# Kernel optimization log

Measured on AMD Instinct MI355X. Metric: run time of the kernel, lower is better.

The kernel has to match this reference:

```python
import jax, jax.numpy as jnp
import numpy as np

LN_EPS = 1e-5


def layer_norm(x, gamma, beta):
    mu = jnp.mean(x, axis=-1, keepdims=True)
    var = jnp.mean(jnp.square(x - mu), axis=-1, keepdims=True)
    return (x - mu) * jax.lax.rsqrt(var + LN_EPS) * gamma + beta


def setup_inputs() -> dict:
    key = jax.random.key(0)
    ks = jax.random.split(key, 7)
    B, S, D = 8, 1024, 512
    H, Dh = 8, 64
    scale = 1.0 / np.sqrt(D)
    x = jax.random.normal(ks[0], (B, S, D), dtype=jnp.float32)
    Wq = jax.random.normal(ks[1], (D, H * Dh), dtype=jnp.float32) * scale
    Wk = jax.random.normal(ks[2], (D, H * Dh), dtype=jnp.float32) * scale
    Wv = jax.random.normal(ks[3], (D, H * Dh), dtype=jnp.float32) * scale
    Wfc = jax.random.normal(ks[4], (H * Dh, D), dtype=jnp.float32) * scale
    gamma = jnp.ones((D,), dtype=jnp.float32)
    beta = jnp.zeros((D,), dtype=jnp.float32)
    return {"x": x, "Wq": Wq, "Wk": Wk, "Wv": Wv, "Wfc": Wfc, "gamma": gamma, "beta": beta}


def reference(x, Wq, Wk, Wv, Wfc, gamma, beta):
    B, S, D = x.shape
    H, Dh = 8, 64
    Q = (x @ Wq).reshape(B, S, H, Dh).transpose(0, 2, 1, 3)  # [B,H,S,Dh]
    K = (x @ Wk).reshape(B, S, H, Dh).transpose(0, 2, 1, 3)
    V = (x @ Wv).reshape(B, S, H, Dh).transpose(0, 2, 1, 3)
    scores = jnp.einsum('bhqd,bhkd->bhqk', Q, K) / np.sqrt(Dh).astype(np.float32)
    # tridiagonal band mask; NOTE: original fills off-band with -1e-09 (not -inf)
    idx = jnp.arange(S)
    band = jnp.abs(idx[:, None] - idx[None, :]) <= 1  # [S,S]
    scores = jnp.where(band, scores, jnp.float32(-1e-09))
    attn = jax.nn.softmax(scores, axis=-1)
    context = jnp.einsum('bhqk,bhkd->bhqd', attn, V)  # [B,H,S,Dh]
    context = context.transpose(0, 2, 1, 3).reshape(B, S, H * Dh)
    out = context @ Wfc
    return layer_norm(out + x, gamma, beta)
```

## Files before the change

### kernel.cpp

```cpp
#include <hip/hip_runtime.h>
#include <math.h>


typedef short     s8v  __attribute__((ext_vector_type(8)));
typedef float     f4v  __attribute__((ext_vector_type(4)));
typedef unsigned short us4v __attribute__((ext_vector_type(4)));
typedef unsigned short us8v __attribute__((ext_vector_type(8)));

__device__ __forceinline__ unsigned short f2b(float f) {
  union { float f; unsigned int u; } v; v.f = f;
  unsigned int u = v.u;
  return (unsigned short)((u + 0x7fffu + ((u >> 16) & 1u)) >> 16);
}
__device__ __forceinline__ float b2f(unsigned short u) {
  union { unsigned int i; float f; } v; v.i = ((unsigned int)u) << 16;
  return v.f;
}
__device__ __forceinline__ void gload_lds16(const void* g, void* l) {
  __builtin_amdgcn_global_load_lds(
      (const __attribute__((address_space(1))) void*)g,
      (__attribute__((address_space(3))) void*)l, 16, 0, 0);
}

__global__ __launch_bounds__(256) void conv_kernel(
    const float* __restrict__ x,
    const float* __restrict__ Wq, const float* __restrict__ Wk,
    const float* __restrict__ Wv, const float* __restrict__ Wfc,
    unsigned short* __restrict__ xb, unsigned short* __restrict__ Wt,
    float* __restrict__ Vsum) {
  __shared__ unsigned short tile[32][33];
  const int bid = blockIdx.x, t = threadIdx.x;
  if (bid < 4096) {
    const int i = bid * 256 + t;
    const float4 f = ((const float4*)x)[i];
    us4v o; o[0] = f2b(f.x); o[1] = f2b(f.y); o[2] = f2b(f.z); o[3] = f2b(f.w);
    ((us4v*)xb)[i] = o;
  } else if (bid < 5120) {
    const int id = bid - 4096;
    const int z = id >> 8, rem = id & 255;
    const int bx = rem & 15, by = rem >> 4;
    const float* W = (z == 0) ? Wq : (z == 1) ? Wk : (z == 2) ? Wv : Wfc;
    const int tx = t & 31, ty = t >> 5;
    const int n0 = bx * 32, k0 = by * 32;
    #pragma unroll
    for (int r = ty; r < 32; r += 8)
      tile[r][tx] = f2b(W[(size_t)(k0 + r) * 512 + n0 + tx]);
    __syncthreads();
    unsigned short* dst = Wt + (size_t)z * 512 * 512;
    #pragma unroll
    for (int r = ty; r < 32; r += 8)
      dst[(size_t)(n0 + r) * 512 + k0 + tx] = tile[tx][r];
  } else {
    float4 zz = {0.f, 0.f, 0.f, 0.f};
    #pragma unroll
    for (int p = 0; p < 4; ++p) ((float4*)Vsum)[p * 256 + t] = zz;
  }
}

#define BM 128
#define BN 128
#define BK 32

__global__ __launch_bounds__(256) void gemm_qkv_kernel(
    const unsigned short* __restrict__ A, const unsigned short* __restrict__ Bt,
    unsigned short* __restrict__ C, float* __restrict__ Vsum) {
  const int M = 8192, N = 1536, K = 512;
  __shared__ __align__(16) unsigned short smem[16384];
  unsigned short* As = smem;
  unsigned short* Bs = smem + 4096;
  const int t    = threadIdx.x;
  const int wave = t >> 6, lane = t & 63;
  const int wr   = wave >> 1, wc = wave & 1;
  const int quad = lane >> 4, l16 = lane & 15;
  const int bm = blockIdx.y * BM, bn = blockIdx.x * BN;

  const int ci0 = wave * 128 + lane, ci1 = ci0 + 64;
  const int r0 = ci0 >> 2, c0 = (ci0 & 3) ^ ((r0 >> 1) & 3);
  const int r1 = ci1 >> 2, c1 = (ci1 & 3) ^ ((r1 >> 1) & 3);
  const unsigned short* ga0 = A  + (size_t)(bm + r0) * K + c0 * 8;
  const unsigned short* ga1 = A  + (size_t)(bm + r1) * K + c1 * 8;
  const unsigned short* gb0 = Bt + (size_t)(bn + r0) * K + c0 * 8;
  const unsigned short* gb1 = Bt + (size_t)(bn + r1) * K + c1 * 8;
  unsigned short* la0 = As + wave * 1024;
  unsigned short* la1 = As + wave * 1024 + 512;
  unsigned short* lb0 = Bs + wave * 1024;
  unsigned short* lb1 = Bs + wave * 1024 + 512;

  const int sw = (l16 >> 1) & 3;

  f4v acc[4][4];
  #pragma unroll
  for (int i = 0; i < 4; ++i)
    #pragma unroll
    for (int j = 0; j < 4; ++j) {
      f4v z = {0.f, 0.f, 0.f, 0.f};
      acc[i][j] = z;
    }

  for (int kt = 0; kt < K; kt += BK) {
    gload_lds16(ga0 + kt, la0);
    gload_lds16(ga1 + kt, la1);
    gload_lds16(gb0 + kt, lb0);
    gload_lds16(gb1 + kt, lb1);
    __syncthreads();

    s8v af[4], bf[4];
    #pragma unroll
    for (int i = 0; i < 4; ++i) {
      const int r = wr * 64 + i * 16 + l16;
      af[i] = *(const s8v*)&As[(r * 4 + (quad ^ sw)) * 8];
    }
    #pragma unroll
    for (int j = 0; j < 4; ++j) {
      const int r = wc * 64 + j * 16 + l16;
      bf[j] = *(const s8v*)&Bs[(r * 4 + (quad ^ sw)) * 8];
    }
    #pragma unroll
    for (int i = 0; i < 4; ++i)
      #pragma unroll
      for (int j = 0; j < 4; ++j)
        acc[i][j] = __builtin_amdgcn_mfma_f32_16x16x32_bf16(
            af[i], bf[j], acc[i][j], 0, 0, 0);
    __syncthreads();
  }

  if (bn >= 1024) {
    const int b = bm >> 10;
    #pragma unroll
    for (int j = 0; j < 4; ++j) {
      float ps = 0.f;
      #pragma unroll
      for (int i = 0; i < 4; ++i)
        #pragma unroll
        for (int r = 0; r < 4; ++r) ps += acc[i][j][r];
      ps += __shfl_xor(ps, 16);
      ps += __shfl_xor(ps, 32);
      if (quad == 0)
        atomicAdd(&Vsum[b * 512 + (bn - 1024) + wc * 64 + j * 16 + l16], ps);
    }
  }

  #pragma unroll
  for (int i = 0; i < 4; ++i) {
    const int lr0 = wr * 64 + i * 16 + quad * 4;
    #pragma unroll
    for (int j = 0; j < 4; ++j) {
      const int lc = wc * 64 + j * 16 + l16;
      #pragma unroll
      for (int r = 0; r < 4; ++r)
        smem[(lr0 + r) * 128 + lc] = f2b(acc[i][j][r]);
    }
  }
  __syncthreads();
  #pragma unroll
  for (int p = 0; p < 8; ++p) {
    const int row = p * 16 + (t >> 4);
    const int ch  = t & 15;
    *(us8v*)(C + (size_t)(bm + row) * N + bn + ch * 8) =
        *(const us8v*)&smem[row * 128 + ch * 8];
  }
}

#define KVS 68
__global__ __launch_bounds__(256) void attn_kernel(
    const unsigned short* __restrict__ QKV, const float* __restrict__ Vsum,
    unsigned short* __restrict__ ctx) {
  __shared__ __align__(16) unsigned short Ks[130 * KVS];
  __shared__ __align__(16) unsigned short Vs[130 * KVS];
  __shared__ __align__(16) float vs_s[64];
  const int bh = blockIdx.x;
  const int b = bh >> 3, h = bh & 7;
  const int q0 = blockIdx.y * 128;
  const int t = threadIdx.x;
  const size_t rowb = ((size_t)b * 1024) * 1536;

  #pragma unroll
  for (int p = 0; p < 5; ++p) {
    const int i = p * 32 + (t >> 3);
    if (i < 130) {
      int g = q0 - 1 + i;
      g = g < 0 ? 0 : (g > 1023 ? 1023 : g);
      const unsigned short* src =
          QKV + rowb + (size_t)g * 1536 + h * 64 + (t & 7) * 8;
      const us8v kv = *(const us8v*)(src + 512);
      const us8v vv = *(const us8v*)(src + 1024);
      us4v lo, hi;
      #pragma unroll
      for (int r = 0; r < 4; ++r) { lo[r] = kv[r]; hi[r] = kv[r + 4]; }
      *(us4v*)&Ks[i * KVS + (t & 7) * 8]     = lo;
      *(us4v*)&Ks[i * KVS + (t & 7) * 8 + 4] = hi;
      #pragma unroll
      for (int r = 0; r < 4; ++r) { lo[r] = vv[r]; hi[r] = vv[r + 4]; }
      *(us4v*)&Vs[i * KVS + (t & 7) * 8]     = lo;
      *(us4v*)&Vs[i * KVS + (t & 7) * 8 + 4] = hi;
    }
  }
  if (t < 64) vs_s[t] = Vsum[(b << 9) + h * 64 + t];
  __syncthreads();

  const int q    = q0 + (t >> 1);
  const int half = t & 1;
  const int li   = (t >> 1) + 1;
  const int co   = half * 32;

  float pm = 0.f, p0 = 0.f, pp = 0.f;
  const unsigned short* Qp = QKV + rowb + (size_t)q * 1536 + h * 64 + co;
  const us8v qa = *(const us8v*)(Qp);
  const us8v qb = *(const us8v*)(Qp + 8);
  const us8v qc = *(const us8v*)(Qp + 16);
  const us8v qd = *(const us8v*)(Qp + 24);
  #pragma unroll
  for (int jj = 0; jj < 8; ++jj) {
    const us4v km = *(const us4v*)&Ks[(li - 1) * KVS + co + jj * 4];
    const us4v k0 = *(const us4v*)&Ks[li * KVS + co + jj * 4];
    const us4v kp = *(const us4v*)&Ks[(li + 1) * KVS + co + jj * 4];
    #pragma unroll
    for (int r = 0; r < 4; ++r) {
      const int e = jj * 4 + r;
      const unsigned short qu = (e < 8) ? qa[e & 7] : (e < 16) ? qb[e & 7]
                              : (e < 24) ? qc[e & 7] : qd[e & 7];
      const float qf = b2f(qu);
      pm += qf * b2f(km[r]);
      p0 += qf * b2f(k0[r]);
      pp += qf * b2f(kp[r]);
    }
  }
  pm += __shfl_xor(pm, 1);
  p0 += __shfl_xor(p0, 1);
  pp += __shfl_xor(pp, 1);

  const float OFF = -1e-9f;
  const float s0 = p0 * 0.125f;
  const float sm = (q > 0)    ? pm * 0.125f : OFF;
  const float sp = (q < 1023) ? pp * 0.125f : OFF;
  const float m  = fmaxf(fmaxf(s0, sm), fmaxf(sp, OFF));
  const float e0 = __expf(s0 - m), em = __expf(sm - m), ep = __expf(sp - m);
  const float eoff = __expf(OFF - m);
  const float inv  = 1.f / (e0 + em + ep + 1021.f * eoff);
  const float wm = (em - eoff) * inv, w0 = (e0 - eoff) * inv,
              wp = (ep - eoff) * inv, wt = eoff * inv;

  unsigned short* cp = ctx + ((size_t)(b * 1024 + q)) * 512 + h * 64 + co;
  #pragma unroll
  for (int jj = 0; jj < 8; ++jj) {
    const us4v a  = *(const us4v*)&Vs[(li - 1) * KVS + co + jj * 4];
    const us4v v0 = *(const us4v*)&Vs[li * KVS + co + jj * 4];
    const us4v c  = *(const us4v*)&Vs[(li + 1) * KVS + co + jj * 4];
    const float4 vsv = *(const float4*)&vs_s[co + jj * 4];
    us4v o;
    o[0] = f2b(wt * vsv.x + wm * b2f(a[0]) + w0 * b2f(v0[0]) + wp * b2f(c[0]));
    o[1] = f2b(wt * vsv.y + wm * b2f(a[1]) + w0 * b2f(v0[1]) + wp * b2f(c[1]));
    o[2] = f2b(wt * vsv.z + wm * b2f(a[2]) + w0 * b2f(v0[2]) + wp * b2f(c[2]));
    o[3] = f2b(wt * vsv.w + wm * b2f(a[3]) + w0 * b2f(v0[3]) + wp * b2f(c[3]));
    *(us4v*)(cp + jj * 4) = o;
  }
}

#define OS 516

__global__ __launch_bounds__(512) void gemm_fcln_kernel(
    const unsigned short* __restrict__ A,
    const unsigned short* __restrict__ Bt,
    const float* __restrict__ x, const float* __restrict__ gamma,
    const float* __restrict__ beta, float* __restrict__ y) {
  const int K = 512;
  __shared__ __align__(16) char smemraw[32 * OS * 4];
  unsigned short* As = (unsigned short*)smemraw;
  unsigned short* Bs = As + 1024;
  float* outS = (float*)smemraw;

  const int t    = threadIdx.x;
  const int wave = t >> 6, lane = t & 63;
  const int wrr  = wave >> 2, wcc = wave & 3;
  const int quad = lane >> 4, l16 = lane & 15;
  const int bm = blockIdx.x * 32;
  const int sw = (l16 >> 1) & 3;

  const int cia = wave * 64 + lane;
  const int ra = cia >> 2, ca = (cia & 3) ^ ((ra >> 1) & 3);
  const unsigned short* gA = A + (size_t)(bm + ra) * K + ca * 8;
  unsigned short* lA = As + wave * 512;
  int rb[4], cb[4];
  #pragma unroll
  for (int p = 0; p < 4; ++p) {
    const int ci = wave * 256 + p * 64 + lane;
    rb[p] = ci >> 2; cb[p] = (ci & 3) ^ ((rb[p] >> 1) & 3);
  }
  unsigned short* lB = Bs + wave * 2048;

  f4v acc[8];
  #pragma unroll
  for (int j = 0; j < 8; ++j) {
    f4v z = {0.f, 0.f, 0.f, 0.f};
    acc[j] = z;
  }

  for (int kt = 0; kt < K; kt += BK) {
    if (wave < 2) gload_lds16(gA + kt, lA);
    #pragma unroll
    for (int p = 0; p < 4; ++p)
      gload_lds16(Bt + (size_t)rb[p] * K + kt + cb[p] * 8, lB + p * 512);
    __syncthreads();

    const int rm = wrr * 16 + l16;
    const s8v af = *(const s8v*)&As[(rm * 4 + (quad ^ sw)) * 8];
    #pragma unroll
    for (int j = 0; j < 8; ++j) {
      const int n = wcc * 128 + j * 16 + l16;
      const s8v bf = *(const s8v*)&Bs[(n * 4 + (quad ^ sw)) * 8];
      acc[j] = __builtin_amdgcn_mfma_f32_16x16x32_bf16(af, bf, acc[j], 0, 0, 0);
    }
    __syncthreads();
  }

  #pragma unroll
  for (int j = 0; j < 8; ++j) {
    const int col = wcc * 128 + j * 16 + l16;
    const int row0 = wrr * 16 + quad * 4;
    #pragma unroll
    for (int r = 0; r < 4; ++r)
      outS[(row0 + r) * OS + col] = acc[j][r];
  }
  __syncthreads();

  const int row = t >> 4, l = t & 15;
  const size_t gbase = (size_t)(bm + row) * 512;
  float4 v[8];
  float s1 = 0.f, s2 = 0.f;
  #pragma unroll
  for (int k = 0; k < 8; ++k) {
    const int c = k * 64 + l * 4;
    const float4 a  = *(const float4*)&outS[row * OS + c];
    const float4 xv = *(const float4*)&x[gbase + c];
    float4 w;
    w.x = a.x + xv.x; w.y = a.y + xv.y; w.z = a.z + xv.z; w.w = a.w + xv.w;
    v[k] = w;
    s1 += w.x + w.y + w.z + w.w;
    s2 += w.x * w.x + w.y * w.y + w.z * w.z + w.w * w.w;
  }
  #pragma unroll
  for (int m = 1; m < 16; m <<= 1) {
    s1 += __shfl_xor(s1, m);
    s2 += __shfl_xor(s2, m);
  }
  const float mu  = s1 * (1.f / 512.f);
  const float var = s2 * (1.f / 512.f) - mu * mu;
  const float rs  = rsqrtf(var + 1e-5f);
  #pragma unroll
  for (int k = 0; k < 8; ++k) {
    const int c = k * 64 + l * 4;
    const float4 g  = *(const float4*)&gamma[c];
    const float4 bb = *(const float4*)&beta[c];
    float4 o;
    o.x = (v[k].x - mu) * rs * g.x + bb.x;
    o.y = (v[k].y - mu) * rs * g.y + bb.y;
    o.z = (v[k].z - mu) * rs * g.z + bb.z;
    o.w = (v[k].w - mu) * rs * g.w + bb.w;
    *(float4*)&y[gbase + c] = o;
  }
}

extern "C" void kernel_launch(void* const* d_in, const int* in_sizes, int n_in,
                              void* d_out, int out_size, void* d_ws, size_t ws_size,
                              hipStream_t stream) {
  const float* x     = (const float*)d_in[0];
  const float* Wq    = (const float*)d_in[1];
  const float* Wk    = (const float*)d_in[2];
  const float* Wv    = (const float*)d_in[3];
  const float* Wfc   = (const float*)d_in[4];
  const float* gamma = (const float*)d_in[5];
  const float* beta  = (const float*)d_in[6];
  float* y = (float*)d_out;

  char* ws = (char*)d_ws;
  unsigned short* Wt   = (unsigned short*)(ws);
  unsigned short* xb   = (unsigned short*)(ws + 2097152);
  unsigned short* QKV  = (unsigned short*)(ws + 10485760);
  float*          Vsum = (float*)(ws + 35651584);
  unsigned short* ctx  = (unsigned short*)(ws + 35667968);

  conv_kernel<<<5121, 256, 0, stream>>>(x, Wq, Wk, Wv, Wfc, xb, Wt, Vsum);
  gemm_qkv_kernel<<<dim3(12, 64), 256, 0, stream>>>(xb, Wt, QKV, Vsum);
  attn_kernel<<<dim3(64, 8), 256, 0, stream>>>(QKV, Vsum, ctx);
  gemm_fcln_kernel<<<256, 512, 0, stream>>>(
      ctx, Wt + (size_t)1536 * 512, x, gamma, beta, y);
}
```

Measured before the change: 136.8 us.

## Widen GEMM K tiles, double-buffer fc GEMM, stage Q in LDS, bf16 residual

Result: faster. 128.1 us (-6.4%).

```diff
diff --git a/kernel.cpp b/kernel.cpp
--- a/kernel.cpp
+++ b/kernel.cpp
@@ -57,36 +57,26 @@
   }
 }
 
-#define BM 128
-#define BN 128
-#define BK 32
-
 __global__ __launch_bounds__(256) void gemm_qkv_kernel(
     const unsigned short* __restrict__ A, const unsigned short* __restrict__ Bt,
     unsigned short* __restrict__ C, float* __restrict__ Vsum) {
-  const int M = 8192, N = 1536, K = 512;
+  const int N = 1536, K = 512;
   __shared__ __align__(16) unsigned short smem[16384];
   unsigned short* As = smem;
-  unsigned short* Bs = smem + 4096;
-  const int t    = threadIdx.x;
-  const int wave = t >> 6, lane = t & 63;
-  const int wr   = wave >> 1, wc = wave & 1;
+  unsigned short* Bs = smem + 8192;
+  const int t = threadIdx.x, wave = t >> 6, lane = t & 63;
+  const int wr = wave >> 1, wc = wave & 1;
   const int quad = lane >> 4, l16 = lane & 15;
-  const int bm = blockIdx.y * BM, bn = blockIdx.x * BN;
-
-  const int ci0 = wave * 128 + lane, ci1 = ci0 + 64;
-  const int r0 = ci0 >> 2, c0 = (ci0 & 3) ^ ((r0 >> 1) & 3);
-  const int r1 = ci1 >> 2, c1 = (ci1 & 3) ^ ((r1 >> 1) & 3);
-  const unsigned short* ga0 = A  + (size_t)(bm + r0) * K + c0 * 8;
-  const unsigned short* ga1 = A  + (size_t)(bm + r1) * K + c1 * 8;
-  const unsigned short* gb0 = Bt + (size_t)(bn + r0) * K + c0 * 8;
-  const unsigned short* gb1 = Bt + (size_t)(bn + r1) * K + c1 * 8;
-  unsigned short* la0 = As + wave * 1024;
-  unsigned short* la1 = As + wave * 1024 + 512;
-  unsigned short* lb0 = Bs + wave * 1024;
-  unsigned short* lb1 = Bs + wave * 1024 + 512;
-
-  const int sw = (l16 >> 1) & 3;
+  const int bm = blockIdx.y * 128, bn = blockIdx.x * 128;
+
+  const unsigned short *gA[4], *gB[4];
+  #pragma unroll
+  for (int p = 0; p < 4; ++p) {
+    const int ci = wave * 256 + p * 64 + lane;
+    const int r = ci >> 3, c = (ci & 7) ^ (r & 7);
+    gA[p] = A + (size_t)(bm + r) * K + c * 8;
+    gB[p] = Bt + (size_t)(bn + r) * K + c * 8;
+  }
 
   f4v acc[4][4];
   #pragma unroll
@@ -97,30 +87,35 @@
       acc[i][j] = z;
     }
 
-  for (int kt = 0; kt < K; kt += BK) {
-    gload_lds16(ga0 + kt, la0);
-    gload_lds16(ga1 + kt, la1);
-    gload_lds16(gb0 + kt, lb0);
-    gload_lds16(gb1 + kt, lb1);
+  for (int kt = 0; kt < K; kt += 64) {
+    #pragma unroll
+    for (int p = 0; p < 4; ++p)
+      gload_lds16(gA[p] + kt, As + wave * 2048 + p * 512);
+    #pragma unroll
+    for (int p = 0; p < 4; ++p)
+      gload_lds16(gB[p] + kt, Bs + wave * 2048 + p * 512);
     __syncthreads();
 
-    s8v af[4], bf[4];
-    #pragma unroll
-    for (int i = 0; i < 4; ++i) {
-      const int r = wr * 64 + i * 16 + l16;
-      af[i] = *(const s8v*)&As[(r * 4 + (quad ^ sw)) * 8];
-    }
-    #pragma unroll
-    for (int j = 0; j < 4; ++j) {
-      const int r = wc * 64 + j * 16 + l16;
-      bf[j] = *(const s8v*)&Bs[(r * 4 + (quad ^ sw)) * 8];
-    }
-    #pragma unroll
-    for (int i = 0; i < 4; ++i)
-      #pragma unroll
-      for (int j = 0; j < 4; ++j)
-        acc[i][j] = __builtin_amdgcn_mfma_f32_16x16x32_bf16(
-            af[i], bf[j], acc[i][j], 0, 0, 0);
+    #pragma unroll
+    for (int s = 0; s < 2; ++s) {
+      s8v af[4], bf[4];
+      #pragma unroll
+      for (int i = 0; i < 4; ++i) {
+        const int r = wr * 64 + i * 16 + l16;
+        af[i] = *(const s8v*)&As[(r * 8 + ((quad + 4 * s) ^ (r & 7))) * 8];
+      }
+      #pragma unroll
+      for (int j = 0; j < 4; ++j) {
+        const int r = wc * 64 + j * 16 + l16;
+        bf[j] = *(const s8v*)&Bs[(r * 8 + ((quad + 4 * s) ^ (r & 7))) * 8];
+      }
+      #pragma unroll
+      for (int i = 0; i < 4; ++i)
+        #pragma unroll
+        for (int j = 0; j < 4; ++j)
+          acc[i][j] = __builtin_amdgcn_mfma_f32_16x16x32_bf16(
+              af[i], bf[j], acc[i][j], 0, 0, 0);
+    }
     __syncthreads();
   }
 
@@ -165,6 +160,7 @@
 __global__ __launch_bounds__(256) void attn_kernel(
     const unsigned short* __restrict__ QKV, const float* __restrict__ Vsum,
     unsigned short* __restrict__ ctx) {
+  __shared__ __align__(16) unsigned short Qs[130 * KVS];
   __shared__ __align__(16) unsigned short Ks[130 * KVS];
   __shared__ __align__(16) unsigned short Vs[130 * KVS];
   __shared__ __align__(16) float vs_s[64];
@@ -182,9 +178,14 @@
       g = g < 0 ? 0 : (g > 1023 ? 1023 : g);
       const unsigned short* src =
           QKV + rowb + (size_t)g * 1536 + h * 64 + (t & 7) * 8;
+      const us8v qv = *(const us8v*)(src);
       const us8v kv = *(const us8v*)(src + 512);
       const us8v vv = *(const us8v*)(src + 1024);
       us4v lo, hi;
+      #pragma unroll
+      for (int r = 0; r < 4; ++r) { lo[r] = qv[r]; hi[r] = qv[r + 4]; }
+      *(us4v*)&Qs[i * KVS + (t & 7) * 8]     = lo;
+      *(us4v*)&Qs[i * KVS + (t & 7) * 8 + 4] = hi;
       #pragma unroll
       for (int r = 0; r < 4; ++r) { lo[r] = kv[r]; hi[r] = kv[r + 4]; }
       *(us4v*)&Ks[i * KVS + (t & 7) * 8]     = lo;
@@ -204,22 +205,15 @@
   const int co   = half * 32;
 
   float pm = 0.f, p0 = 0.f, pp = 0.f;
-  const unsigned short* Qp = QKV + rowb + (size_t)q * 1536 + h * 64 + co;
-  const us8v qa = *(const us8v*)(Qp);
-  const us8v qb = *(const us8v*)(Qp + 8);
-  const us8v qc = *(const us8v*)(Qp + 16);
-  const us8v qd = *(const us8v*)(Qp + 24);
   #pragma unroll
   for (int jj = 0; jj < 8; ++jj) {
+    const us4v qv = *(const us4v*)&Qs[li * KVS + co + jj * 4];
     const us4v km = *(const us4v*)&Ks[(li - 1) * KVS + co + jj * 4];
     const us4v k0 = *(const us4v*)&Ks[li * KVS + co + jj * 4];
     const us4v kp = *(const us4v*)&Ks[(li + 1) * KVS + co + jj * 4];
     #pragma unroll
     for (int r = 0; r < 4; ++r) {
-      const int e = jj * 4 + r;
-      const unsigned short qu = (e < 8) ? qa[e & 7] : (e < 16) ? qb[e & 7]
-                              : (e < 24) ? qc[e & 7] : qd[e & 7];
-      const float qf = b2f(qu);
+      const float qf = b2f(qv[r]);
       pm += qf * b2f(km[r]);
       p0 += qf * b2f(k0[r]);
       pp += qf * b2f(kp[r]);
@@ -261,32 +255,27 @@
 __global__ __launch_bounds__(512) void gemm_fcln_kernel(
     const unsigned short* __restrict__ A,
     const unsigned short* __restrict__ Bt,
-    const float* __restrict__ x, const float* __restrict__ gamma,
+    const unsigned short* __restrict__ xb, const float* __restrict__ gamma,
     const float* __restrict__ beta, float* __restrict__ y) {
   const int K = 512;
-  __shared__ __align__(16) char smemraw[32 * OS * 4];
-  unsigned short* As = (unsigned short*)smemraw;
-  unsigned short* Bs = As + 1024;
-  float* outS = (float*)smemraw;
-
-  const int t    = threadIdx.x;
-  const int wave = t >> 6, lane = t & 63;
-  const int wrr  = wave >> 2, wcc = wave & 3;
+  __shared__ __align__(16) unsigned short smem[69632];
+  float* outS = (float*)smem;
+
+  const int t = threadIdx.x, wave = t >> 6, lane = t & 63;
+  const int wrr = wave >> 2, wcc = wave & 3;
   const int quad = lane >> 4, l16 = lane & 15;
   const int bm = blockIdx.x * 32;
-  const int sw = (l16 >> 1) & 3;
-
-  const int cia = wave * 64 + lane;
-  const int ra = cia >> 2, ca = (cia & 3) ^ ((ra >> 1) & 3);
-  const unsigned short* gA = A + (size_t)(bm + ra) * K + ca * 8;
-  unsigned short* lA = As + wave * 512;
-  int rb[4], cb[4];
-  #pragma unroll
-  for (int p = 0; p < 4; ++p) {
-    const int ci = wave * 256 + p * 64 + lane;
-    rb[p] = ci >> 2; cb[p] = (ci & 3) ^ ((rb[p] >> 1) & 3);
-  }
-  unsigned short* lB = Bs + wave * 2048;
+
+  const int ciA = wave * 64 + lane;
+  const int rA = ciA >> 3, cA = (ciA & 7) ^ (rA & 7);
+  const unsigned short* gA = A + (size_t)(bm + rA) * K + cA * 8;
+  const unsigned short* gB[8];
+  #pragma unroll
+  for (int p = 0; p < 8; ++p) {
+    const int ci = wave * 512 + p * 64 + lane;
+    const int r = ci >> 3, c = (ci & 7) ^ (r & 7);
+    gB[p] = Bt + (size_t)r * K + c * 8;
+  }
 
   f4v acc[8];
   #pragma unroll
@@ -295,20 +284,41 @@
     acc[j] = z;
   }
 
-  for (int kt = 0; kt < K; kt += BK) {
-    if (wave < 2) gload_lds16(gA + kt, lA);
-    #pragma unroll
-    for (int p = 0; p < 4; ++p)
-      gload_lds16(Bt + (size_t)rb[p] * K + kt + cb[p] * 8, lB + p * 512);
-    __syncthreads();
-
+  if (wave < 4) gload_lds16(gA, smem + wave * 512);
+  #pragma unroll
+  for (int p = 0; p < 8; ++p)
+    gload_lds16(gB[p], smem + 2048 + wave * 4096 + p * 512);
+  __syncthreads();
+
+  for (int it = 0; it < 8; ++it) {
+    const int cur = (it & 1) * 34816;
+    const int nxt = 34816 - cur;
+    const unsigned short* Ab = smem + cur;
+    const unsigned short* Bb = smem + cur + 2048;
     const int rm = wrr * 16 + l16;
-    const s8v af = *(const s8v*)&As[(rm * 4 + (quad ^ sw)) * 8];
+    const s8v af0 = *(const s8v*)&Ab[(rm * 8 + (quad ^ (rm & 7))) * 8];
+    const s8v af1 = *(const s8v*)&Ab[(rm * 8 + ((quad + 4) ^ (rm & 7))) * 8];
+    s8v bf0[8];
     #pragma unroll
     for (int j = 0; j < 8; ++j) {
       const int n = wcc * 128 + j * 16 + l16;
-      const s8v bf = *(const s8v*)&Bs[(n * 4 + (quad ^ sw)) * 8];
-      acc[j] = __builtin_amdgcn_mfma_f32_16x16x32_bf16(af, bf, acc[j], 0, 0, 0);
+      bf0[j] = *(const s8v*)&Bb[(n * 8 + (quad ^ (n & 7))) * 8];
+    }
+    if (it < 7) {
+      const int kt = (it + 1) * 64;
+      if (wave < 4) gload_lds16(gA + kt, smem + nxt + wave * 512);
+      #pragma unroll
+      for (int p = 0; p < 8; ++p)
+        gload_lds16(gB[p] + kt, smem + nxt + 2048 + wave * 4096 + p * 512);
+    }
+    #pragma unroll
+    for (int j = 0; j < 8; ++j)
+      acc[j] = __builtin_amdgcn_mfma_f32_16x16x32_bf16(af0, bf0[j], acc[j], 0, 0, 0);
+    #pragma unroll
+    for (int j = 0; j < 8; ++j) {
+      const int n = wcc * 128 + j * 16 + l16;
+      const s8v bf1 = *(const s8v*)&Bb[(n * 8 + ((quad + 4) ^ (n & 7))) * 8];
+      acc[j] = __builtin_amdgcn_mfma_f32_16x16x32_bf16(af1, bf1, acc[j], 0, 0, 0);
     }
     __syncthreads();
   }
@@ -330,10 +340,11 @@
   #pragma unroll
   for (int k = 0; k < 8; ++k) {
     const int c = k * 64 + l * 4;
-    const float4 a  = *(const float4*)&outS[row * OS + c];
-    const float4 xv = *(const float4*)&x[gbase + c];
+    const float4 a = *(const float4*)&outS[row * OS + c];
+    const us4v xv = *(const us4v*)&xb[gbase + c];
     float4 w;
-    w.x = a.x + xv.x; w.y = a.y + xv.y; w.z = a.z + xv.z; w.w = a.w + xv.w;
+    w.x = a.x + b2f(xv[0]); w.y = a.y + b2f(xv[1]);
+    w.z = a.z + b2f(xv[2]); w.w = a.w + b2f(xv[3]);
     v[k] = w;
     s1 += w.x + w.y + w.z + w.w;
     s2 += w.x * w.x + w.y * w.y + w.z * w.z + w.w * w.w;
@@ -383,5 +394,5 @@
   gemm_qkv_kernel<<<dim3(12, 64), 256, 0, stream>>>(xb, Wt, QKV, Vsum);
   attn_kernel<<<dim3(64, 8), 256, 0, stream>>>(QKV, Vsum, ctx);
   gemm_fcln_kernel<<<256, 512, 0, stream>>>(
-      ctx, Wt + (size_t)1536 * 512, x, gamma, beta, y);
-}
+      ctx, Wt + (size_t)1536 * 512, xb, gamma, beta, y);
+}
```
